# Kernel optimization log

Measured on AMD Instinct MI355X. Metric: run time of the kernel, lower is better.

## Reference

```python
import jax, jax.numpy as jnp
import numpy as np

HIDDEN = 2048
HEADS = 16
HEAD_DIM = HIDDEN // HEADS
TOP_K = 256
B, N = 1, 2048


def setup_inputs() -> dict:
    key = jax.random.key(0)
    ks = jax.random.split(key, 9)
    s = 0.02
    return {
        "hidden_states": jax.random.normal(ks[0], (B, N, HIDDEN), jnp.float32),
        "Wq": jax.random.normal(ks[1], (HIDDEN, HIDDEN), jnp.float32) * s,
        "bq": jnp.zeros((HIDDEN,), jnp.float32),
        "Wk": jax.random.normal(ks[2], (HIDDEN, HIDDEN), jnp.float32) * s,
        "bk": jnp.zeros((HIDDEN,), jnp.float32),
        "Wv": jax.random.normal(ks[3], (HIDDEN, HIDDEN), jnp.float32) * s,
        "bv": jnp.zeros((HIDDEN,), jnp.float32),
        "Wo": jax.random.normal(ks[4], (HIDDEN, HIDDEN), jnp.float32) * s,
        "bo": jnp.zeros((HIDDEN,), jnp.float32),
    }


def _split_heads(x):
    b, n, _ = x.shape
    return x.reshape(b, n, HEADS, HEAD_DIM).transpose(0, 2, 1, 3)  # b h n d


def reference(hidden_states, Wq, bq, Wk, bk, Wv, bv, Wo, bo):
    scale = 1.0 / jnp.sqrt(jnp.float32(HEAD_DIM))
    q = _split_heads(hidden_states @ Wq + bq)  # [b,h,n,d]
    k = _split_heads(hidden_states @ Wk + bk)
    v = _split_heads(hidden_states @ Wv + bv)

    # Sparse path (kv_seq_length > attention_window): dense QK^T used only to rank keys.
    scores = jnp.einsum("bhnd,bhmd->bhnm", q, k) * scale  # [b,h,n,n]
    importance = scores.mean(axis=2)  # [b,h,n] aggregate over queries
    _, idx = jax.lax.top_k(importance, TOP_K)  # [b,h,k]

    # gather selected K/V (torch.gather along seq dim)
    k_sel = jnp.take_along_axis(k, idx[..., None], axis=2)  # [b,h,k,d]
    v_sel = jnp.take_along_axis(v, idx[..., None], axis=2)

    w = jax.nn.softmax(jnp.einsum("bhnd,bhkd->bhnk", q, k_sel) * scale, axis=-1)
    out = jnp.einsum("bhnk,bhkd->bhnd", w, v_sel)  # [b,h,n,d]
    out = out.transpose(0, 2, 1, 3).reshape(hidden_states.shape[0], -1, HIDDEN)
    return out @ Wo + bo
```

## Files before the change

kernel.cpp:

```cpp
#include <hip/hip_runtime.h>


typedef __attribute__((ext_vector_type(8))) short bf16x8;
typedef __attribute__((ext_vector_type(4))) float f32x4;

__device__ __forceinline__ unsigned short f2bf(float x) {
    unsigned u = __float_as_uint(x);
    u += 0x7fffu + ((u >> 16) & 1u);
    return (unsigned short)(u >> 16);
}

__device__ __forceinline__ void load_lds16(const unsigned short* g, unsigned short* l) {
    __builtin_amdgcn_global_load_lds(
        (const __attribute__((address_space(1))) unsigned int*)g,
        (__attribute__((address_space(3))) unsigned int*)l,
        16, 0, 0);
}

struct Bias3 { const float* p0; const float* p1; const float* p2; };
struct Ptr4  { const float* p[4]; };

template <int TN, bool OUT_BF16>
__global__ __launch_bounds__(256) void gemm_bf16(
    const unsigned short* __restrict__ A, long lda, long strideA,
    const unsigned short* __restrict__ Bt, long ldb, long strideB,
    void* __restrict__ Cv, long ldc, long strideC,
    Bias3 bias, int K, float alpha)
{
    constexpr int SN = TN / 32;
    __shared__ __align__(16) unsigned short As[128][32];
    __shared__ __align__(16) unsigned short Bs[TN][32];

    const int tid  = threadIdx.x;
    const int lane = tid & 63;
    const int wave = tid >> 6;
    const int wm = wave >> 1, wn = wave & 1;

    const int bm = blockIdx.y * 128;
    const int bn = blockIdx.x * TN;
    const int b  = blockIdx.z;

    const unsigned short* Ab = A  + (long)b * strideA;
    const unsigned short* Bb = Bt + (long)b * strideB;

    f32x4 acc[4][SN];
#pragma unroll
    for (int i = 0; i < 4; i++)
#pragma unroll
        for (int j = 0; j < SN; j++) acc[i][j] = f32x4{0.f, 0.f, 0.f, 0.f};

    const int lr = lane >> 2;
    const int lc = (lane & 3) * 8;

    for (int k0 = 0; k0 < K; k0 += 32) {
        __syncthreads();
#pragma unroll
        for (int r0 = wave * 16; r0 < 128; r0 += 64)
            load_lds16(Ab + (long)(bm + r0 + lr) * lda + k0 + lc, &As[r0][0]);
#pragma unroll
        for (int r0 = wave * 16; r0 < TN; r0 += 64)
            load_lds16(Bb + (long)(bn + r0 + lr) * ldb + k0 + lc, &Bs[r0][0]);
        __syncthreads();

        bf16x8 af[4], bf[SN];
#pragma unroll
        for (int s = 0; s < 4; s++)
            af[s] = *(const bf16x8*)&As[wm * 64 + s * 16 + (lane & 15)][(lane >> 4) * 8];
#pragma unroll
        for (int t = 0; t < SN; t++)
            bf[t] = *(const bf16x8*)&Bs[wn * (TN / 2) + t * 16 + (lane & 15)][(lane >> 4) * 8];
#pragma unroll
        for (int s = 0; s < 4; s++)
#pragma unroll
            for (int t = 0; t < SN; t++)
                acc[s][t] = __builtin_amdgcn_mfma_f32_16x16x32_bf16(af[s], bf[t], acc[s][t], 0, 0, 0);
    }

    const float* bp = (b == 0) ? bias.p0 : (b == 1) ? bias.p1 : bias.p2;
    float* Cf = (float*)Cv;
    unsigned short* Ch = (unsigned short*)Cv;
#pragma unroll
    for (int s = 0; s < 4; s++) {
#pragma unroll
        for (int t = 0; t < SN; t++) {
            const int col  = bn + wn * (TN / 2) + t * 16 + (lane & 15);
            const int row0 = bm + wm * 64 + s * 16 + (lane >> 4) * 4;
            const float bv = bp ? bp[col] : 0.f;
#pragma unroll
            for (int r = 0; r < 4; r++) {
                float v = alpha * acc[s][t][r] + bv;
                long off = (long)b * strideC + (long)(row0 + r) * ldc + col;
                if (OUT_BF16) Ch[off] = f2bf(v);
                else          Cf[off] = v;
            }
        }
    }
}

__global__ __launch_bounds__(256, 1) void attn_kernel(
    const unsigned short* __restrict__ Qb,
    const unsigned short* __restrict__ Ksel,
    const unsigned short* __restrict__ VselT,
    unsigned short* __restrict__ Att)
{
    __shared__ __align__(16) unsigned short Qs[128][32];
    __shared__ __align__(16) unsigned short Ks[256][32];
    __shared__ __align__(16) unsigned short Vs[128][32];
    __shared__ __align__(16) unsigned short Ps[128][264];
    __shared__ float linv[128];

    const int tid  = threadIdx.x;
    const int lane = tid & 63;
    const int wave = tid >> 6;
    const int bm = blockIdx.x * 128;
    const int h  = blockIdx.y;
    const int lr = lane >> 2, lc = (lane & 3) * 8;

    const unsigned short* Kh = Ksel  + h * 32768;
    const unsigned short* Vh = VselT + h * 32768;

    f32x4 acc[2][16];
#pragma unroll
    for (int s = 0; s < 2; s++)
#pragma unroll
        for (int t = 0; t < 16; t++) acc[s][t] = f32x4{0.f, 0.f, 0.f, 0.f};

    for (int k0 = 0; k0 < 128; k0 += 32) {
        __syncthreads();
#pragma unroll
        for (int r0 = wave * 16; r0 < 128; r0 += 64)
            load_lds16(Qb + (long)(bm + r0 + lr) * 2048 + h * 128 + k0 + lc, &Qs[r0][0]);
#pragma unroll
        for (int r0 = wave * 16; r0 < 256; r0 += 64)
            load_lds16(Kh + (r0 + lr) * 128 + k0 + lc, &Ks[r0][0]);
        __syncthreads();

        bf16x8 af[2];
#pragma unroll
        for (int s = 0; s < 2; s++)
            af[s] = *(const bf16x8*)&Qs[wave * 32 + s * 16 + (lane & 15)][(lane >> 4) * 8];
#pragma unroll
        for (int t = 0; t < 16; t++) {
            bf16x8 bf = *(const bf16x8*)&Ks[t * 16 + (lane & 15)][(lane >> 4) * 8];
            acc[0][t] = __builtin_amdgcn_mfma_f32_16x16x32_bf16(af[0], bf, acc[0][t], 0, 0, 0);
            acc[1][t] = __builtin_amdgcn_mfma_f32_16x16x32_bf16(af[1], bf, acc[1][t], 0, 0, 0);
        }
    }

    const float se = 0.08838834764831845f * 1.4426950408889634f;
#pragma unroll
    for (int s = 0; s < 2; s++) {
#pragma unroll
        for (int r = 0; r < 4; r++) {
            float mx = -3.0e38f;
#pragma unroll
            for (int t = 0; t < 16; t++) mx = fmaxf(mx, acc[s][t][r]);
#pragma unroll
            for (int off = 1; off < 16; off <<= 1) mx = fmaxf(mx, __shfl_xor(mx, off));
            float sum = 0.f;
#pragma unroll
            for (int t = 0; t < 16; t++) {
                float p = exp2f((acc[s][t][r] - mx) * se);
                acc[s][t][r] = p;
                sum += p;
            }
#pragma unroll
            for (int off = 1; off < 16; off <<= 1) sum += __shfl_xor(sum, off);
            const int row = wave * 32 + s * 16 + (lane >> 4) * 4 + r;
#pragma unroll
            for (int t = 0; t < 16; t++)
                Ps[row][t * 16 + (lane & 15)] = f2bf(acc[s][t][r]);
            if ((lane & 15) == 0) linv[row] = 1.0f / sum;
        }
    }

    const int wm2 = wave >> 1, wn2 = wave & 1;
    f32x4 acc2[4][4];
#pragma unroll
    for (int i = 0; i < 4; i++)
#pragma unroll
        for (int j = 0; j < 4; j++) acc2[i][j] = f32x4{0.f, 0.f, 0.f, 0.f};

    for (int j0 = 0; j0 < 256; j0 += 32) {
        __syncthreads();
#pragma unroll
        for (int r0 = wave * 16; r0 < 128; r0 += 64)
            load_lds16(Vh + (r0 + lr) * 256 + j0 + lc, &Vs[r0][0]);
        __syncthreads();

        bf16x8 af2[4], bf2[4];
#pragma unroll
        for (int s2 = 0; s2 < 4; s2++)
            af2[s2] = *(const bf16x8*)&Ps[wm2 * 64 + s2 * 16 + (lane & 15)][j0 + (lane >> 4) * 8];
#pragma unroll
        for (int t2 = 0; t2 < 4; t2++)
            bf2[t2] = *(const bf16x8*)&Vs[wn2 * 64 + t2 * 16 + (lane & 15)][(lane >> 4) * 8];
#pragma unroll
        for (int s2 = 0; s2 < 4; s2++)
#pragma unroll
            for (int t2 = 0; t2 < 4; t2++)
                acc2[s2][t2] = __builtin_amdgcn_mfma_f32_16x16x32_bf16(af2[s2], bf2[t2], acc2[s2][t2], 0, 0, 0);
    }

#pragma unroll
    for (int s2 = 0; s2 < 4; s2++) {
#pragma unroll
        for (int t2 = 0; t2 < 4; t2++) {
            const int d = wn2 * 64 + t2 * 16 + (lane & 15);
#pragma unroll
            for (int r = 0; r < 4; r++) {
                const int row = wm2 * 64 + s2 * 16 + (lane >> 4) * 4 + r;
                float v = acc2[s2][t2][r] * linv[row];
                Att[(long)(bm + row) * 2048 + h * 128 + d] = f2bf(v);
            }
        }
    }
}

__global__ void transpose_cast4(Ptr4 srcs, unsigned short* __restrict__ WT4) {
    __shared__ float tile[32][33];
    const float* W = srcs.p[blockIdx.z];
    unsigned short* WT = WT4 + (long)blockIdx.z * 4194304;
    const int bx = blockIdx.x * 32;
    const int by = blockIdx.y * 32;
    const int x = threadIdx.x, y = threadIdx.y;
#pragma unroll
    for (int i = 0; i < 32; i += 8)
        tile[y + i][x] = W[(long)(by + y + i) * 2048 + bx + x];
    __syncthreads();
#pragma unroll
    for (int i = 0; i < 32; i += 8)
        WT[(long)(bx + y + i) * 2048 + by + x] = f2bf(tile[x][y + i]);
}

__global__ void fill_kernel(float* p, float v, long n) {
    long i = ((long)blockIdx.x * blockDim.x + threadIdx.x) * 4;
    if (i + 3 < n) { p[i] = v; p[i+1] = v; p[i+2] = v; p[i+3] = v; }
}

__global__ __launch_bounds__(256) void colsum_part(const float* __restrict__ hs,
                                                   double* __restrict__ part) {
    const int col = blockIdx.x * 256 + threadIdx.x;
    const int r0  = blockIdx.y * 32;
    double a = 0.0;
#pragma unroll 4
    for (int r = 0; r < 32; r++) a += (double)hs[(long)(r0 + r) * 2048 + col];
    part[(long)blockIdx.y * 2048 + col] = a;
}

__global__ void colsum_fin(const double* __restrict__ part, float* __restrict__ hsbar) {
    const int col = blockIdx.x * 64 + threadIdx.x;
    double s = 0.0;
#pragma unroll 4
    for (int g = 0; g < 64; g++) s += part[(long)g * 2048 + col];
    hsbar[col] = (float)(s * (1.0 / 2048.0));
}

__global__ __launch_bounds__(256) void qsum_part(const float* __restrict__ hsbar,
                                                 const float* __restrict__ Wq,
                                                 double* __restrict__ partq) {
    const int j  = blockIdx.x * 256 + threadIdx.x;
    const int i0 = blockIdx.y * 32;
    double a = 0.0;
#pragma unroll 4
    for (int r = 0; r < 32; r++)
        a += (double)hsbar[i0 + r] * (double)Wq[(long)(i0 + r) * 2048 + j];
    partq[(long)blockIdx.y * 2048 + j] = a;
}

__global__ void qsum_fin(const double* __restrict__ partq, const float* __restrict__ bq,
                         float* __restrict__ qbar) {
    const int j = blockIdx.x * 64 + threadIdx.x;
    double s = (double)bq[j];
#pragma unroll 4
    for (int g = 0; g < 64; g++) s += partq[(long)g * 2048 + j];
    qbar[j] = (float)s;
}

__global__ __launch_bounds__(256) void u_kernel(const float* __restrict__ Wk,
                                                const float* __restrict__ qbar,
                                                float* __restrict__ U) {
    const int i = blockIdx.x, t = threadIdx.x;
#pragma unroll
    for (int r = 0; r < 2; r++) {
        const int e = r * 1024 + t * 4;
        float4 w = *(const float4*)(Wk + (long)i * 2048 + e);
        float4 q = *(const float4*)(qbar + e);
        float a = w.x * q.x + w.y * q.y + w.z * q.z + w.w * q.w;
#pragma unroll
        for (int off = 16; off; off >>= 1) a += __shfl_xor(a, off);
        if ((t & 31) == 0) U[(long)i * 16 + r * 8 + (t >> 5)] = a;
    }
}

__global__ __launch_bounds__(256) void cast_imp_kernel(const float* __restrict__ hs,
                                                       const float* __restrict__ U,
                                                       unsigned short* __restrict__ HSb,
                                                       float* __restrict__ imp) {
    __shared__ float row[2048];
    __shared__ float red[4][16];
    const int m = blockIdx.x, t = threadIdx.x;
    for (int i = t; i < 2048; i += 256) {
        float v = hs[(long)m * 2048 + i];
        row[i] = v;
        HSb[(long)m * 2048 + i] = f2bf(v);
    }
    __syncthreads();
    float p[16];
#pragma unroll
    for (int h = 0; h < 16; h++) p[h] = 0.f;
    for (int i = t * 8; i < t * 8 + 8; i++) {
        const float v = row[i];
        const float* u = U + i * 16;
#pragma unroll
        for (int h = 0; h < 16; h++) p[h] += v * u[h];
    }
#pragma unroll
    for (int off = 32; off; off >>= 1)
#pragma unroll
        for (int h = 0; h < 16; h++) p[h] += __shfl_down(p[h], off);
    if ((t & 63) == 0)
#pragma unroll
        for (int h = 0; h < 16; h++) red[t >> 6][h] = p[h];
    __syncthreads();
    if (t < 16)
        imp[(long)t * 2048 + m] = red[0][t] + red[1][t] + red[2][t] + red[3][t];
}

__global__ __launch_bounds__(64) void topk_kernel(const float* __restrict__ imp,
                                                  int* __restrict__ idx) {
    const int h = blockIdx.x;
    const int lane = threadIdx.x;
    unsigned u[32];
#pragma unroll
    for (int r = 0; r < 32; r++) {
        unsigned x = __float_as_uint(imp[(long)h * 2048 + r * 64 + lane]);
        u[r] = (x & 0x80000000u) ? ~x : (x | 0x80000000u);
    }
    unsigned cur = 0;
    for (int b = 31; b >= 0; b--) {
        const unsigned cand = cur | (1u << b);
        int tot = 0;
#pragma unroll
        for (int r = 0; r < 32; r++)
            tot += (int)__popcll(__ballot(u[r] >= cand));
        if (tot >= 256) cur = cand;
    }
    const unsigned long long below = (1ull << lane) - 1ull;
    int base = 0;
#pragma unroll
    for (int r = 0; r < 32; r++) {
        const bool q = u[r] > cur;
        const unsigned long long m = __ballot(q);
        if (q) idx[h * 256 + base + (int)__popcll(m & below)] = r * 64 + lane;
        base += (int)__popcll(m);
    }
#pragma unroll
    for (int r = 0; r < 32; r++) {
        const bool q = (u[r] == cur);
        const unsigned long long m = __ballot(q);
        if (q) {
            const int pos = base + (int)__popcll(m & below);
            if (pos < 256) idx[h * 256 + pos] = r * 64 + lane;
        }
        base += (int)__popcll(m);
        if (base >= 256) break;
    }
}

__global__ void gather_kernel(const unsigned short* __restrict__ Kb,
                              const unsigned short* __restrict__ Vb,
                              const int* __restrict__ idx,
                              unsigned short* __restrict__ Ksel,
                              unsigned short* __restrict__ VselT) {
    int t = blockIdx.x * blockDim.x + threadIdx.x;
    {
        int d = t & 127, j = (t >> 7) & 255, h = t >> 15;
        int sr = idx[h * 256 + j];
        Ksel[t] = Kb[(long)sr * 2048 + h * 128 + d];
    }
    {
        int j = t & 255, d = (t >> 8) & 127, h = t >> 15;
        int sr = idx[h * 256 + j];
        VselT[t] = Vb[(long)sr * 2048 + h * 128 + d];
    }
}

extern "C" void kernel_launch(void* const* d_in, const int* in_sizes, int n_in,
                              void* d_out, int out_size, void* d_ws, size_t ws_size,
                              hipStream_t stream)
{
    const float* hs = (const float*)d_in[0];
    const float* Wq = (const float*)d_in[1];
    const float* bq = (const float*)d_in[2];
    const float* Wk = (const float*)d_in[3];
    const float* bk = (const float*)d_in[4];
    const float* Wv = (const float*)d_in[5];
    const float* bv = (const float*)d_in[6];
    const float* Wo = (const float*)d_in[7];
    const float* bo = (const float*)d_in[8];

    char* ws = (char*)d_ws;
    size_t off = 0;
    auto alloc = [&](size_t b) -> void* {
        void* p = ws + off;
        off = (off + b + 255) & ~(size_t)255;
        return p;
    };
    unsigned short* HSb   = (unsigned short*)alloc(8388608);
    unsigned short* WT4   = (unsigned short*)alloc(4 * 8388608);
    unsigned short* QKVb  = (unsigned short*)alloc(3 * 8388608);
    unsigned short* Att   = (unsigned short*)alloc(8388608);
    unsigned short* Ksel  = (unsigned short*)alloc(1048576);
    unsigned short* VselT = (unsigned short*)alloc(1048576);
    double* part  = (double*)alloc(1048576);
    float* hsbar = (float*)alloc(8192);
    float* qbar  = (float*)alloc(8192);
    float* U     = (float*)alloc(131072);
    float* imp   = (float*)alloc(131072);
    int*   idx   = (int*)alloc(16384);

    if (off > ws_size) {
        fill_kernel<<<4096, 256, 0, stream>>>((float*)d_out, 12345.0f, (long)out_size);
        return;
    }

    unsigned short* Qb = QKVb;
    unsigned short* Kb = QKVb + 4194304;
    unsigned short* Vb = QKVb + 2 * 4194304;
    unsigned short* WoT = WT4 + 3 * 4194304;

    transpose_cast4<<<dim3(64, 64, 4), dim3(32, 8), 0, stream>>>(Ptr4{{Wq, Wk, Wv, Wo}}, WT4);

    colsum_part<<<dim3(8, 64), 256, 0, stream>>>(hs, part);
    colsum_fin<<<32, 64, 0, stream>>>(part, hsbar);
    qsum_part<<<dim3(8, 64), 256, 0, stream>>>(hsbar, Wq, part);
    qsum_fin<<<32, 64, 0, stream>>>(part, bq, qbar);
    u_kernel<<<2048, 256, 0, stream>>>(Wk, qbar, U);
    cast_imp_kernel<<<2048, 256, 0, stream>>>(hs, U, HSb, imp);
    topk_kernel<<<16, 64, 0, stream>>>(imp, idx);

    gemm_bf16<128, true><<<dim3(16, 16, 3), 256, 0, stream>>>(
        HSb, 2048, 0, WT4, 2048, 4194304, QKVb, 2048, 4194304,
        Bias3{bq, bk, bv}, 2048, 1.0f);

    gather_kernel<<<2048, 256, 0, stream>>>(Kb, Vb, idx, Ksel, VselT);

    attn_kernel<<<dim3(16, 16), 256, 0, stream>>>(Qb, Ksel, VselT, Att);

    gemm_bf16<64, false><<<dim3(32, 16, 1), 256, 0, stream>>>(
        Att, 2048, 0, WoT, 2048, 0, d_out, 2048, 0,
        Bias3{bo, bo, bo}, 2048, 1.0f);
}
```

Measured before the change: 338.1 us.

## Fuse prep kernels, merge topk with gather, halve attention query tile

Merges the weight transpose/cast and the column-sum partial into one launch, and folds the column-mean finalisation into the Wq projection partial. It also fuses top-k selection with the K/V gather, using an LDS-staged transpose for V. The attention kernel now uses 64-row query tiles with launch bounds allowing two blocks per CU, doubling the grid from 256 to 512 blocks. The aim is fewer launches and better occupancy, at the cost of the gather running on only 16 blocks and K being re-read per query tile.

```diff
diff --git a/kernel.cpp b/kernel.cpp
--- a/kernel.cpp
+++ b/kernel.cpp
@@ -97,119 +97,111 @@
     }
 }
 
-__global__ __launch_bounds__(256, 1) void attn_kernel(
+__global__ __launch_bounds__(256, 2) void attn_kernel(
     const unsigned short* __restrict__ Qb,
     const unsigned short* __restrict__ Ksel,
     const unsigned short* __restrict__ VselT,
     unsigned short* __restrict__ Att)
 {
-    __shared__ __align__(16) unsigned short Qs[128][32];
+    __shared__ __align__(16) unsigned short Qs[64][32];
     __shared__ __align__(16) unsigned short Ks[256][32];
     __shared__ __align__(16) unsigned short Vs[128][32];
-    __shared__ __align__(16) unsigned short Ps[128][264];
-    __shared__ float linv[128];
+    __shared__ __align__(16) unsigned short Ps[64][264];
+    __shared__ float linv[64];
 
     const int tid  = threadIdx.x;
     const int lane = tid & 63;
     const int wave = tid >> 6;
-    const int bm = blockIdx.x * 128;
+    const int bm = blockIdx.x * 64;
     const int h  = blockIdx.y;
     const int lr = lane >> 2, lc = (lane & 3) * 8;
 
     const unsigned short* Kh = Ksel  + h * 32768;
     const unsigned short* Vh = VselT + h * 32768;
 
-    f32x4 acc[2][16];
-#pragma unroll
-    for (int s = 0; s < 2; s++)
-#pragma unroll
-        for (int t = 0; t < 16; t++) acc[s][t] = f32x4{0.f, 0.f, 0.f, 0.f};
+    f32x4 acc[16];
+#pragma unroll
+    for (int t = 0; t < 16; t++) acc[t] = f32x4{0.f, 0.f, 0.f, 0.f};
 
     for (int k0 = 0; k0 < 128; k0 += 32) {
         __syncthreads();
-#pragma unroll
-        for (int r0 = wave * 16; r0 < 128; r0 += 64)
-            load_lds16(Qb + (long)(bm + r0 + lr) * 2048 + h * 128 + k0 + lc, &Qs[r0][0]);
-#pragma unroll
-        for (int r0 = wave * 16; r0 < 256; r0 += 64)
-            load_lds16(Kh + (r0 + lr) * 128 + k0 + lc, &Ks[r0][0]);
-        __syncthreads();
-
-        bf16x8 af[2];
-#pragma unroll
-        for (int s = 0; s < 2; s++)
-            af[s] = *(const bf16x8*)&Qs[wave * 32 + s * 16 + (lane & 15)][(lane >> 4) * 8];
+        load_lds16(Qb + (long)(bm + wave * 16 + lr) * 2048 + h * 128 + k0 + lc,
+                   &Qs[wave * 16][0]);
+#pragma unroll
+        for (int q = 0; q < 4; q++)
+            load_lds16(Kh + (wave * 64 + q * 16 + lr) * 128 + k0 + lc,
+                       &Ks[wave * 64 + q * 16][0]);
+        __syncthreads();
+
+        bf16x8 af = *(const bf16x8*)&Qs[wave * 16 + (lane & 15)][(lane >> 4) * 8];
 #pragma unroll
         for (int t = 0; t < 16; t++) {
-            bf16x8 bf = *(const bf16x8*)&Ks[t * 16 + (lane & 15)][(lane >> 4) * 8];
-            acc[0][t] = __builtin_amdgcn_mfma_f32_16x16x32_bf16(af[0], bf, acc[0][t], 0, 0, 0);
-            acc[1][t] = __builtin_amdgcn_mfma_f32_16x16x32_bf16(af[1], bf, acc[1][t], 0, 0, 0);
+            bf16x8 bfv = *(const bf16x8*)&Ks[t * 16 + (lane & 15)][(lane >> 4) * 8];
+            acc[t] = __builtin_amdgcn_mfma_f32_16x16x32_bf16(af, bfv, acc[t], 0, 0, 0);
         }
     }
 
     const float se = 0.08838834764831845f * 1.4426950408889634f;
 #pragma unroll
-    for (int s = 0; s < 2; s++) {
-#pragma unroll
-        for (int r = 0; r < 4; r++) {
-            float mx = -3.0e38f;
-#pragma unroll
-            for (int t = 0; t < 16; t++) mx = fmaxf(mx, acc[s][t][r]);
-#pragma unroll
-            for (int off = 1; off < 16; off <<= 1) mx = fmaxf(mx, __shfl_xor(mx, off));
-            float sum = 0.f;
-#pragma unroll
-            for (int t = 0; t < 16; t++) {
-                float p = exp2f((acc[s][t][r] - mx) * se);
-                acc[s][t][r] = p;
-                sum += p;
-            }
-#pragma unroll
-            for (int off = 1; off < 16; off <<= 1) sum += __shfl_xor(sum, off);
-            const int row = wave * 32 + s * 16 + (lane >> 4) * 4 + r;
-#pragma unroll
-            for (int t = 0; t < 16; t++)
-                Ps[row][t * 16 + (lane & 15)] = f2bf(acc[s][t][r]);
-            if ((lane & 15) == 0) linv[row] = 1.0f / sum;
-        }
+    for (int r = 0; r < 4; r++) {
+        float mx = -3.0e38f;
+#pragma unroll
+        for (int t = 0; t < 16; t++) mx = fmaxf(mx, acc[t][r]);
+#pragma unroll
+        for (int off = 1; off < 16; off <<= 1) mx = fmaxf(mx, __shfl_xor(mx, off));
+        float sum = 0.f;
+#pragma unroll
+        for (int t = 0; t < 16; t++) {
+            float p = exp2f((acc[t][r] - mx) * se);
+            acc[t][r] = p;
+            sum += p;
+        }
+#pragma unroll
+        for (int off = 1; off < 16; off <<= 1) sum += __shfl_xor(sum, off);
+        const int row = wave * 16 + (lane >> 4) * 4 + r;
+#pragma unroll
+        for (int t = 0; t < 16; t++)
+            Ps[row][t * 16 + (lane & 15)] = f2bf(acc[t][r]);
+        if ((lane & 15) == 0) linv[row] = 1.0f / sum;
     }
 
     const int wm2 = wave >> 1, wn2 = wave & 1;
-    f32x4 acc2[4][4];
-#pragma unroll
-    for (int i = 0; i < 4; i++)
+    f32x4 acc2[2][4];
+#pragma unroll
+    for (int i = 0; i < 2; i++)
 #pragma unroll
         for (int j = 0; j < 4; j++) acc2[i][j] = f32x4{0.f, 0.f, 0.f, 0.f};
 
     for (int j0 = 0; j0 < 256; j0 += 32) {
         __syncthreads();
 #pragma unroll
-        for (int r0 = wave * 16; r0 < 128; r0 += 64)
-            load_lds16(Vh + (r0 + lr) * 256 + j0 + lc, &Vs[r0][0]);
-        __syncthreads();
-
-        bf16x8 af2[4], bf2[4];
-#pragma unroll
-        for (int s2 = 0; s2 < 4; s2++)
-            af2[s2] = *(const bf16x8*)&Ps[wm2 * 64 + s2 * 16 + (lane & 15)][j0 + (lane >> 4) * 8];
+        for (int q = 0; q < 2; q++)
+            load_lds16(Vh + (wave * 32 + q * 16 + lr) * 256 + j0 + lc,
+                       &Vs[wave * 32 + q * 16][0]);
+        __syncthreads();
+
+        bf16x8 af2[2], bf2v[4];
+#pragma unroll
+        for (int s2 = 0; s2 < 2; s2++)
+            af2[s2] = *(const bf16x8*)&Ps[wm2 * 32 + s2 * 16 + (lane & 15)][j0 + (lane >> 4) * 8];
 #pragma unroll
         for (int t2 = 0; t2 < 4; t2++)
-            bf2[t2] = *(const bf16x8*)&Vs[wn2 * 64 + t2 * 16 + (lane & 15)][(lane >> 4) * 8];
-#pragma unroll
-        for (int s2 = 0; s2 < 4; s2++)
+            bf2v[t2] = *(const bf16x8*)&Vs[wn2 * 64 + t2 * 16 + (lane & 15)][(lane >> 4) * 8];
+#pragma unroll
+        for (int s2 = 0; s2 < 2; s2++)
 #pragma unroll
             for (int t2 = 0; t2 < 4; t2++)
-                acc2[s2][t2] = __builtin_amdgcn_mfma_f32_16x16x32_bf16(af2[s2], bf2[t2], acc2[s2][t2], 0, 0, 0);
-    }
-
-#pragma unroll
-    for (int s2 = 0; s2 < 4; s2++) {
+                acc2[s2][t2] = __builtin_amdgcn_mfma_f32_16x16x32_bf16(af2[s2], bf2v[t2], acc2[s2][t2], 0, 0, 0);
+    }
+
+#pragma unroll
+    for (int s2 = 0; s2 < 2; s2++) {
 #pragma unroll
         for (int t2 = 0; t2 < 4; t2++) {
             const int d = wn2 * 64 + t2 * 16 + (lane & 15);
 #pragma unroll
             for (int r = 0; r < 4; r++) {
-                const int row = wm2 * 64 + s2 * 16 + (lane >> 4) * 4 + r;
+                const int row = wm2 * 32 + s2 * 16 + (lane >> 4) * 4 + r;
                 float v = acc2[s2][t2][r] * linv[row];
                 Att[(long)(bm + row) * 2048 + h * 128 + d] = f2bf(v);
             }
@@ -217,20 +209,35 @@
     }
 }
 
-__global__ void transpose_cast4(Ptr4 srcs, unsigned short* __restrict__ WT4) {
-    __shared__ float tile[32][33];
-    const float* W = srcs.p[blockIdx.z];
-    unsigned short* WT = WT4 + (long)blockIdx.z * 4194304;
-    const int bx = blockIdx.x * 32;
-    const int by = blockIdx.y * 32;
-    const int x = threadIdx.x, y = threadIdx.y;
-#pragma unroll
-    for (int i = 0; i < 32; i += 8)
-        tile[y + i][x] = W[(long)(by + y + i) * 2048 + bx + x];
-    __syncthreads();
-#pragma unroll
-    for (int i = 0; i < 32; i += 8)
-        WT[(long)(bx + y + i) * 2048 + by + x] = f2bf(tile[x][y + i]);
+__global__ __launch_bounds__(256) void prep_kernel(Ptr4 srcs, unsigned short* __restrict__ WT4,
+                                                   const float* __restrict__ hs,
+                                                   double* __restrict__ part) {
+    const int b = blockIdx.x;
+    const int tid = threadIdx.x;
+    if (b < 16384) {
+        __shared__ float tile[32][33];
+        const int z = b >> 12, xy = b & 4095;
+        const float* W = srcs.p[z];
+        unsigned short* WT = WT4 + (long)z * 4194304;
+        const int bx = (xy & 63) * 32;
+        const int by = (xy >> 6) * 32;
+        const int x = tid & 31, y = tid >> 5;
+#pragma unroll
+        for (int i = 0; i < 32; i += 8)
+            tile[y + i][x] = W[(long)(by + y + i) * 2048 + bx + x];
+        __syncthreads();
+#pragma unroll
+        for (int i = 0; i < 32; i += 8)
+            WT[(long)(bx + y + i) * 2048 + by + x] = f2bf(tile[x][y + i]);
+    } else {
+        const int c = b - 16384;
+        const int col = (c & 7) * 256 + tid;
+        const int r0  = (c >> 3) * 32;
+        double a = 0.0;
+#pragma unroll 4
+        for (int r = 0; r < 32; r++) a += (double)hs[(long)(r0 + r) * 2048 + col];
+        part[(long)(c >> 3) * 2048 + col] = a;
+    }
 }
 
 __global__ void fill_kernel(float* p, float v, long n) {
@@ -238,33 +245,23 @@
     if (i + 3 < n) { p[i] = v; p[i+1] = v; p[i+2] = v; p[i+3] = v; }
 }
 
-__global__ __launch_bounds__(256) void colsum_part(const float* __restrict__ hs,
-                                                   double* __restrict__ part) {
-    const int col = blockIdx.x * 256 + threadIdx.x;
-    const int r0  = blockIdx.y * 32;
-    double a = 0.0;
-#pragma unroll 4
-    for (int r = 0; r < 32; r++) a += (double)hs[(long)(r0 + r) * 2048 + col];
-    part[(long)blockIdx.y * 2048 + col] = a;
-}
-
-__global__ void colsum_fin(const double* __restrict__ part, float* __restrict__ hsbar) {
-    const int col = blockIdx.x * 64 + threadIdx.x;
-    double s = 0.0;
-#pragma unroll 4
-    for (int g = 0; g < 64; g++) s += part[(long)g * 2048 + col];
-    hsbar[col] = (float)(s * (1.0 / 2048.0));
-}
-
-__global__ __launch_bounds__(256) void qsum_part(const float* __restrict__ hsbar,
-                                                 const float* __restrict__ Wq,
-                                                 double* __restrict__ partq) {
+__global__ __launch_bounds__(256) void mean_qsum_part(const double* __restrict__ part,
+                                                      const float* __restrict__ Wq,
+                                                      double* __restrict__ partq) {
+    __shared__ float hsb[32];
     const int j  = blockIdx.x * 256 + threadIdx.x;
     const int i0 = blockIdx.y * 32;
+    if (threadIdx.x < 32) {
+        double s = 0.0;
+#pragma unroll 4
+        for (int g = 0; g < 64; g++) s += part[(long)g * 2048 + i0 + threadIdx.x];
+        hsb[threadIdx.x] = (float)(s * (1.0 / 2048.0));
+    }
+    __syncthreads();
     double a = 0.0;
 #pragma unroll 4
     for (int r = 0; r < 32; r++)
-        a += (double)hsbar[i0 + r] * (double)Wq[(long)(i0 + r) * 2048 + j];
+        a += (double)hsb[r] * (double)Wq[(long)(i0 + r) * 2048 + j];
     partq[(long)blockIdx.y * 2048 + j] = a;
 }
 
@@ -327,62 +324,81 @@
         imp[(long)t * 2048 + m] = red[0][t] + red[1][t] + red[2][t] + red[3][t];
 }
 
-__global__ __launch_bounds__(64) void topk_kernel(const float* __restrict__ imp,
-                                                  int* __restrict__ idx) {
+__global__ __launch_bounds__(256) void topk_gather(const float* __restrict__ imp,
+                                                   const unsigned short* __restrict__ Kb,
+                                                   const unsigned short* __restrict__ Vb,
+                                                   unsigned short* __restrict__ Ksel,
+                                                   unsigned short* __restrict__ VselT) {
+    __shared__ int sidx[256];
+    __shared__ unsigned short Vt[64][130];
     const int h = blockIdx.x;
-    const int lane = threadIdx.x;
-    unsigned u[32];
-#pragma unroll
-    for (int r = 0; r < 32; r++) {
-        unsigned x = __float_as_uint(imp[(long)h * 2048 + r * 64 + lane]);
-        u[r] = (x & 0x80000000u) ? ~x : (x | 0x80000000u);
-    }
-    unsigned cur = 0;
-    for (int b = 31; b >= 0; b--) {
-        const unsigned cand = cur | (1u << b);
-        int tot = 0;
-#pragma unroll
-        for (int r = 0; r < 32; r++)
-            tot += (int)__popcll(__ballot(u[r] >= cand));
-        if (tot >= 256) cur = cand;
-    }
-    const unsigned long long below = (1ull << lane) - 1ull;
-    int base = 0;
-#pragma unroll
-    for (int r = 0; r < 32; r++) {
-        const bool q = u[r] > cur;
-        const unsigned long long m = __ballot(q);
-        if (q) idx[h * 256 + base + (int)__popcll(m & below)] = r * 64 + lane;
-        base += (int)__popcll(m);
-    }
-#pragma unroll
-    for (int r = 0; r < 32; r++) {
-        const bool q = (u[r] == cur);
-        const unsigned long long m = __ballot(q);
-        if (q) {
-            const int pos = base + (int)__popcll(m & below);
-            if (pos < 256) idx[h * 256 + pos] = r * 64 + lane;
-        }
-        base += (int)__popcll(m);
-        if (base >= 256) break;
-    }
-}
-
-__global__ void gather_kernel(const unsigned short* __restrict__ Kb,
-                              const unsigned short* __restrict__ Vb,
-                              const int* __restrict__ idx,
-                              unsigned short* __restrict__ Ksel,
-                              unsigned short* __restrict__ VselT) {
-    int t = blockIdx.x * blockDim.x + threadIdx.x;
-    {
-        int d = t & 127, j = (t >> 7) & 255, h = t >> 15;
-        int sr = idx[h * 256 + j];
-        Ksel[t] = Kb[(long)sr * 2048 + h * 128 + d];
-    }
-    {
-        int j = t & 255, d = (t >> 8) & 127, h = t >> 15;
-        int sr = idx[h * 256 + j];
-        VselT[t] = Vb[(long)sr * 2048 + h * 128 + d];
+    const int tid = threadIdx.x;
+    const int lane = tid & 63;
+    const int wave = tid >> 6;
+
+    if (wave == 0) {
+        unsigned u[32];
+#pragma unroll
+        for (int r = 0; r < 32; r++) {
+            unsigned x = __float_as_uint(imp[(long)h * 2048 + r * 64 + lane]);
+            u[r] = (x & 0x80000000u) ? ~x : (x | 0x80000000u);
+        }
+        unsigned cur = 0;
+        for (int b = 31; b >= 0; b--) {
+            const unsigned cand = cur | (1u << b);
+            int tot = 0;
+#pragma unroll
+            for (int r = 0; r < 32; r++)
+                tot += (int)__popcll(__ballot(u[r] >= cand));
+            if (tot >= 256) cur = cand;
+        }
+        const unsigned long long below = (1ull << lane) - 1ull;
+        int base = 0;
+#pragma unroll
+        for (int r = 0; r < 32; r++) {
+            const bool q = u[r] > cur;
+            const unsigned long long m = __ballot(q);
+            if (q) sidx[base + (int)__popcll(m & below)] = r * 64 + lane;
+            base += (int)__popcll(m);
+        }
+#pragma unroll
+        for (int r = 0; r < 32; r++) {
+            const bool q = (u[r] == cur);
+            const unsigned long long m = __ballot(q);
+            if (q) {
+                const int pos = base + (int)__popcll(m & below);
+                if (pos < 256) sidx[pos] = r * 64 + lane;
+            }
+            base += (int)__popcll(m);
+            if (base >= 256) break;
+        }
+    }
+    __syncthreads();
+
+    unsigned short* Kh = Ksel + h * 32768;
+#pragma unroll 4
+    for (int jj = 0; jj < 64; jj++) {
+        const int j = wave * 64 + jj;
+        const long sr = sidx[j];
+        *(ushort2*)&Kh[j * 128 + lane * 2] =
+            *(const ushort2*)&Kb[sr * 2048 + h * 128 + lane * 2];
+    }
+
+    unsigned short* Vh = VselT + h * 32768;
+    for (int j0 = 0; j0 < 256; j0 += 64) {
+        __syncthreads();
+#pragma unroll 4
+        for (int jj = 0; jj < 16; jj++) {
+            const int jl = wave * 16 + jj;
+            const long sr = sidx[j0 + jl];
+            *(ushort2*)&Vt[jl][lane * 2] =
+                *(const ushort2*)&Vb[sr * 2048 + h * 128 + lane * 2];
+        }
+        __syncthreads();
+#pragma unroll 8
+        for (int d = wave; d < 128; d += 4) {
+            Vh[d * 256 + j0 + lane] = Vt[lane][d];
+        }
     }
 }
 
@@ -414,11 +430,10 @@
     unsigned short* Ksel  = (unsigned short*)alloc(1048576);
     unsigned short* VselT = (unsigned short*)alloc(1048576);
     double* part  = (double*)alloc(1048576);
-    float* hsbar = (float*)alloc(8192);
+    double* partq = (double*)alloc(1048576);
     float* qbar  = (float*)alloc(8192);
     float* U     = (float*)alloc(131072);
     float* imp   = (float*)alloc(131072);
-    int*   idx   = (int*)alloc(16384);
 
     if (off > ws_size) {
         fill_kernel<<<4096, 256, 0, stream>>>((float*)d_out, 12345.0f, (long)out_size);
@@ -430,23 +445,20 @@
     unsigned short* Vb = QKVb + 2 * 4194304;
     unsigned short* WoT = WT4 + 3 * 4194304;
 
-    transpose_cast4<<<dim3(64, 64, 4), dim3(32, 8), 0, stream>>>(Ptr4{{Wq, Wk, Wv, Wo}}, WT4);
-
-    colsum_part<<<dim3(8, 64), 256, 0, stream>>>(hs, part);
-    colsum_fin<<<32, 64, 0, stream>>>(part, hsbar);
-    qsum_part<<<dim3(8, 64), 256, 0, stream>>>(hsbar, Wq, part);
-    qsum_fin<<<32, 64, 0, stream>>>(part, bq, qbar);
+    prep_kernel<<<16896, 256, 0, stream>>>(Ptr4{{Wq, Wk, Wv, Wo}}, WT4, hs, part);
+
+    mean_qsum_part<<<dim3(8, 64), 256, 0, stream>>>(part, Wq, partq);
+    qsum_fin<<<32, 64, 0, stream>>>(partq, bq, qbar);
     u_kernel<<<2048, 256, 0, stream>>>(Wk, qbar, U);
     cast_imp_kernel<<<2048, 256, 0, stream>>>(hs, U, HSb, imp);
-    topk_kernel<<<16, 64, 0, stream>>>(imp, idx);
 
     gemm_bf16<128, true><<<dim3(16, 16, 3), 256, 0, stream>>>(
         HSb, 2048, 0, WT4, 2048, 4194304, QKVb, 2048, 4194304,
         Bias3{bq, bk, bv}, 2048, 1.0f);
 
-    gather_kernel<<<2048, 256, 0, stream>>>(Kb, Vb, idx, Ksel, VselT);
-
-    attn_kernel<<<dim3(16, 16), 256, 0, stream>>>(Qb, Ksel, VselT, Att);
+    topk_gather<<<16, 256, 0, stream>>>(imp, Kb, Vb, Ksel, VselT);
+
+    attn_kernel<<<dim3(32, 16), 256, 0, stream>>>(Qb, Ksel, VselT, Att);
 
     gemm_bf16<64, false><<<dim3(32, 16, 1), 256, 0, stream>>>(
         Att, 2048, 0, WoT, 2048, 0, d_out, 2048, 0,
```

New measurement: 335.0 us. About the same (-0.9%).
